# Optimization experiments

Measured on AMD Instinct MI355X. Metric: run time of the kernel, lower is better.

Reference implementation:

```python
import jax, jax.numpy as jnp
from jax import lax
import numpy as np

WIN = 9  # default window [9, 9] in the original module


def _box_sum(x, win):
    """Sum over a win x win window, stride 1, pad win//2 (same as conv2d with ones kernel).
    Implemented separably (two 1D convs) - mathematically identical to the 2D ones-kernel conv.
    x: [B, 1, H, W] float32.
    """
    pad = win // 2
    kh = jnp.ones((1, 1, win, 1), x.dtype)
    kw = jnp.ones((1, 1, 1, win), x.dtype)
    dn = lax.conv_dimension_numbers(x.shape, kh.shape, ('NCHW', 'OIHW', 'NCHW'))
    y = lax.conv_general_dilated(x, kh, (1, 1), [(pad, pad), (0, 0)], dimension_numbers=dn)
    return lax.conv_general_dilated(y, kw, (1, 1), [(0, 0), (pad, pad)], dimension_numbers=dn)


def setup_inputs() -> dict:
    key = jax.random.key(0)
    k1, k2 = jax.random.split(key)
    shape = (32, 1, 512, 512)
    predict = jax.random.uniform(k1, shape, dtype=jnp.float32)
    target = jax.random.uniform(k2, shape, dtype=jnp.float32)
    return {"predict": predict, "target": target}


def reference(predict, target):
    win = WIN
    win_size = jnp.asarray(win * win, jnp.float32)

    I, J = predict, target
    I_sum = _box_sum(I, win)
    J_sum = _box_sum(J, win)
    I2_sum = _box_sum(I * I, win)
    J2_sum = _box_sum(J * J, win)
    IJ_sum = _box_sum(I * J, win)

    u_I = I_sum / win_size
    u_J = J_sum / win_size

    cross = IJ_sum - u_J * I_sum - u_I * J_sum + u_I * u_J * win_size
    I_var = I2_sum - 2.0 * u_I * I_sum + u_I * u_I * win_size
    J_var = J2_sum - 2.0 * u_J * J_sum + u_J * u_J * win_size

    cc = cross * cross / (I_var * J_var + 1e-6)
    return -jnp.mean(cc) + 1.0
```

## Files before the change

### kernel.cpp

```cpp
#include <hip/hip_runtime.h>


#define W 512
#define H 512
#define BH 4
#define NBANDS (H / BH)
#define NT 256
#define WPB 4

__device__ __forceinline__ float4 ld4(const float* p) {
    return *reinterpret_cast<const float4*>(p);
}

#define VROW(row, OP)                                                        \
    do {                                                                     \
        const float* _ip = Ip + (row) * W + x0;                              \
        const float* _jp = Jp + (row) * W + x0;                              \
        float4 _A0 = ld4(_ip);                                               \
        float4 _A1 = ld4(_ip + 4);                                           \
        float4 _B0 = ld4(_jp);                                               \
        float4 _B1 = ld4(_jp + 4);                                           \
        float _a0 = _A0.x, _a1 = _A0.y, _a2 = _A0.z, _a3 = _A0.w;            \
        float _a4 = _A1.x, _a5 = _A1.y, _a6 = _A1.z, _a7 = _A1.w;            \
        float _b0 = _B0.x, _b1 = _B0.y, _b2 = _B0.z, _b3 = _B0.w;            \
        float _b4 = _B1.x, _b5 = _B1.y, _b6 = _B1.z, _b7 = _B1.w;            \
        v0[0] OP _a0; v0[1] OP _a1; v0[2] OP _a2; v0[3] OP _a3;              \
        v0[4] OP _a4; v0[5] OP _a5; v0[6] OP _a6; v0[7] OP _a7;              \
        v1[0] OP _b0; v1[1] OP _b1; v1[2] OP _b2; v1[3] OP _b3;              \
        v1[4] OP _b4; v1[5] OP _b5; v1[6] OP _b6; v1[7] OP _b7;              \
        v2[0] OP _a0*_a0; v2[1] OP _a1*_a1; v2[2] OP _a2*_a2; v2[3] OP _a3*_a3; \
        v2[4] OP _a4*_a4; v2[5] OP _a5*_a5; v2[6] OP _a6*_a6; v2[7] OP _a7*_a7; \
        v3[0] OP _b0*_b0; v3[1] OP _b1*_b1; v3[2] OP _b2*_b2; v3[3] OP _b3*_b3; \
        v3[4] OP _b4*_b4; v3[5] OP _b5*_b5; v3[6] OP _b6*_b6; v3[7] OP _b7*_b7; \
        v4[0] OP _a0*_b0; v4[1] OP _a1*_b1; v4[2] OP _a2*_b2; v4[3] OP _a3*_b3; \
        v4[4] OP _a4*_b4; v4[5] OP _a5*_b5; v4[6] OP _a6*_b6; v4[7] OP _a7*_b7; \
    } while (0)

#define HSUM(vv, h)                                                          \
    do {                                                                     \
        float _l4 = __shfl_up(vv[4], 1),  _l5 = __shfl_up(vv[5], 1);         \
        float _l6 = __shfl_up(vv[6], 1),  _l7 = __shfl_up(vv[7], 1);         \
        float _r0 = __shfl_down(vv[0], 1), _r1 = __shfl_down(vv[1], 1);      \
        float _r2 = __shfl_down(vv[2], 1), _r3 = __shfl_down(vv[3], 1);      \
        _l4 = lane ? _l4 : 0.f; _l5 = lane ? _l5 : 0.f;                      \
        _l6 = lane ? _l6 : 0.f; _l7 = lane ? _l7 : 0.f;                      \
        _r0 = lastl ? 0.f : _r0; _r1 = lastl ? 0.f : _r1;                    \
        _r2 = lastl ? 0.f : _r2; _r3 = lastl ? 0.f : _r3;                    \
        float _t = (((_l4 + _l5) + (_l6 + _l7)) +                            \
                    ((vv[0] + vv[1]) + (vv[2] + vv[3]))) + vv[4];            \
        h[0] = _t;                                                           \
        _t += vv[5] - _l4;  h[1] = _t;                                       \
        _t += vv[6] - _l5;  h[2] = _t;                                       \
        _t += vv[7] - _l6;  h[3] = _t;                                       \
        _t += _r0   - _l7;  h[4] = _t;                                       \
        _t += _r1 - vv[0];  h[5] = _t;                                       \
        _t += _r2 - vv[1];  h[6] = _t;                                       \
        _t += _r3 - vv[2];  h[7] = _t;                                       \
    } while (0)

__global__ __launch_bounds__(NT)
void ncc_main(const float* __restrict__ I, const float* __restrict__ J,
              float* __restrict__ partials) {
    const int lane  = threadIdx.x & 63;
    const bool lastl = (lane == 63);
    const int wid   = threadIdx.x >> 6;

    const int nblk = gridDim.x;
    const int sblk = (blockIdx.x & 7) * (nblk >> 3) + (blockIdx.x >> 3);

    const int g    = sblk * WPB + wid;
    const int b    = g >> 7;
    const int band = g & (NBANDS - 1);
    const int y0   = band * BH;
    const float* Ip = I + (size_t)b * (H * W);
    const float* Jp = J + (size_t)b * (H * W);
    const int x0 = lane * 8;

    float v0[8], v1[8], v2[8], v3[8], v4[8];
    #pragma unroll
    for (int k = 0; k < 8; ++k) { v0[k]=0.f; v1[k]=0.f; v2[k]=0.f; v3[k]=0.f; v4[k]=0.f; }

    #pragma unroll
    for (int dr = -4; dr < 4; ++dr) {
        int r = y0 + dr;
        if (r >= 0) VROW(r, +=);
    }

    float cc_acc = 0.f;
    const float inv81 = 1.f / 81.f;
    #pragma unroll
    for (int i = 0; i < BH; ++i) {
        const int y = y0 + i;
        if (y + 4 < H) VROW(y + 4, +=);

        float h0[8], h1[8], h2[8], h3[8], h4[8];
        HSUM(v0, h0);
        HSUM(v1, h1);
        HSUM(v2, h2);
        HSUM(v3, h3);
        HSUM(v4, h4);

        #pragma unroll
        for (int c = 0; c < 8; ++c) {
            float Is = h0[c], Js = h1[c];
            float I2 = h2[c], J2 = h3[c], IJ = h4[c];
            float u     = Is * inv81;
            float cross = IJ - u * Js;
            float Ivar  = I2 - u * Is;
            float Jvar  = J2 - (Js * inv81) * Js;
            float r     = __builtin_amdgcn_rcpf(Ivar * Jvar + 1e-6f);
            cc_acc += (cross * cross) * r;
        }

        if (y - 4 >= 0) VROW(y - 4, -=);
    }

    #pragma unroll
    for (int off = 32; off > 0; off >>= 1)
        cc_acc += __shfl_down(cc_acc, off, 64);
    __shared__ float wsum[WPB];
    if (lane == 0) wsum[wid] = cc_acc;
    __syncthreads();
    if (threadIdx.x == 0)
        partials[blockIdx.x] = (wsum[0] + wsum[1]) + (wsum[2] + wsum[3]);
}

__global__ __launch_bounds__(256)
void ncc_finish(const float* __restrict__ partials, float* __restrict__ out,
                int n, float inv_total) {
    float v = 0.f;
    for (int i = threadIdx.x; i < n; i += blockDim.x) v += partials[i];
    #pragma unroll
    for (int off = 32; off > 0; off >>= 1)
        v += __shfl_down(v, off, 64);
    __shared__ float wsum[4];
    if ((threadIdx.x & 63) == 0) wsum[threadIdx.x >> 6] = v;
    __syncthreads();
    if (threadIdx.x == 0) {
        float t = (wsum[0] + wsum[1]) + (wsum[2] + wsum[3]);
        out[0] = 1.0f - t * inv_total;
    }
}

extern "C" void kernel_launch(void* const* d_in, const int* in_sizes, int n_in,
                              void* d_out, int out_size, void* d_ws, size_t ws_size,
                              hipStream_t stream) {
    const float* I = (const float*)d_in[0];
    const float* J = (const float*)d_in[1];
    float* out = (float*)d_out;
    float* partials = (float*)d_ws;

    const int n = in_sizes[0];
    const int B = n / (H * W);
    const int nblocks = B * NBANDS / WPB;

    ncc_main<<<nblocks, NT, 0, stream>>>(I, J, partials);
    ncc_finish<<<1, 256, 0, stream>>>(partials, out, nblocks, 1.0f / (float)n);
}
```

Before: 120.0 us.

## Software-pipeline row loads with double buffers and split horizontal sum epilogue

Replaces the conditional per-row load-and-accumulate with an explicit two-buffer software pipeline, so the next row's global loads are issued before the current row is accumulated. Out-of-range rows are clamped to a valid address and masked by a sign multiplier instead of being skipped by a branch. The horizontal sliding sum is split into low and high halves so fewer temporaries stay live, and launch bounds now request 4 blocks per CU. This aims to hide memory latency and lower register pressure, at the cost of extra multiplies and redundant loads on boundary bands.

Result: faster. 116.8 us (-2.7%).

```diff
diff --git a/kernel.cpp b/kernel.cpp
--- a/kernel.cpp
+++ b/kernel.cpp
@@ -12,58 +12,87 @@
     return *reinterpret_cast<const float4*>(p);
 }
 
-#define VROW(row, OP)                                                        \
-    do {                                                                     \
-        const float* _ip = Ip + (row) * W + x0;                              \
-        const float* _jp = Jp + (row) * W + x0;                              \
-        float4 _A0 = ld4(_ip);                                               \
-        float4 _A1 = ld4(_ip + 4);                                           \
-        float4 _B0 = ld4(_jp);                                               \
-        float4 _B1 = ld4(_jp + 4);                                           \
-        float _a0 = _A0.x, _a1 = _A0.y, _a2 = _A0.z, _a3 = _A0.w;            \
-        float _a4 = _A1.x, _a5 = _A1.y, _a6 = _A1.z, _a7 = _A1.w;            \
-        float _b0 = _B0.x, _b1 = _B0.y, _b2 = _B0.z, _b3 = _B0.w;            \
-        float _b4 = _B1.x, _b5 = _B1.y, _b6 = _B1.z, _b7 = _B1.w;            \
-        v0[0] OP _a0; v0[1] OP _a1; v0[2] OP _a2; v0[3] OP _a3;              \
-        v0[4] OP _a4; v0[5] OP _a5; v0[6] OP _a6; v0[7] OP _a7;              \
-        v1[0] OP _b0; v1[1] OP _b1; v1[2] OP _b2; v1[3] OP _b3;              \
-        v1[4] OP _b4; v1[5] OP _b5; v1[6] OP _b6; v1[7] OP _b7;              \
-        v2[0] OP _a0*_a0; v2[1] OP _a1*_a1; v2[2] OP _a2*_a2; v2[3] OP _a3*_a3; \
-        v2[4] OP _a4*_a4; v2[5] OP _a5*_a5; v2[6] OP _a6*_a6; v2[7] OP _a7*_a7; \
-        v3[0] OP _b0*_b0; v3[1] OP _b1*_b1; v3[2] OP _b2*_b2; v3[3] OP _b3*_b3; \
-        v3[4] OP _b4*_b4; v3[5] OP _b5*_b5; v3[6] OP _b6*_b6; v3[7] OP _b7*_b7; \
-        v4[0] OP _a0*_b0; v4[1] OP _a1*_b1; v4[2] OP _a2*_b2; v4[3] OP _a3*_b3; \
-        v4[4] OP _a4*_b4; v4[5] OP _a5*_b5; v4[6] OP _a6*_b6; v4[7] OP _a7*_b7; \
-    } while (0)
+#define DECLBUF(P) float4 P##A0, P##A1, P##B0, P##B1; float P##m
 
-#define HSUM(vv, h)                                                          \
-    do {                                                                     \
-        float _l4 = __shfl_up(vv[4], 1),  _l5 = __shfl_up(vv[5], 1);         \
-        float _l6 = __shfl_up(vv[6], 1),  _l7 = __shfl_up(vv[7], 1);         \
-        float _r0 = __shfl_down(vv[0], 1), _r1 = __shfl_down(vv[1], 1);      \
-        float _r2 = __shfl_down(vv[2], 1), _r3 = __shfl_down(vv[3], 1);      \
-        _l4 = lane ? _l4 : 0.f; _l5 = lane ? _l5 : 0.f;                      \
-        _l6 = lane ? _l6 : 0.f; _l7 = lane ? _l7 : 0.f;                      \
-        _r0 = lastl ? 0.f : _r0; _r1 = lastl ? 0.f : _r1;                    \
-        _r2 = lastl ? 0.f : _r2; _r3 = lastl ? 0.f : _r3;                    \
-        float _t = (((_l4 + _l5) + (_l6 + _l7)) +                            \
-                    ((vv[0] + vv[1]) + (vv[2] + vv[3]))) + vv[4];            \
-        h[0] = _t;                                                           \
-        _t += vv[5] - _l4;  h[1] = _t;                                       \
-        _t += vv[6] - _l5;  h[2] = _t;                                       \
-        _t += vv[7] - _l6;  h[3] = _t;                                       \
-        _t += _r0   - _l7;  h[4] = _t;                                       \
-        _t += _r1 - vv[0];  h[5] = _t;                                       \
-        _t += _r2 - vv[1];  h[6] = _t;                                       \
-        _t += _r3 - vv[2];  h[7] = _t;                                       \
-    } while (0)
+#define PLOAD(P, DRK, SGNK) do {                                             \
+    int _r  = y0 + (DRK);                                                    \
+    int _rc = _r < 0 ? 0 : (_r > (H - 1) ? (H - 1) : _r);                    \
+    const float* _ip = Ip + _rc * W + x0;                                    \
+    const float* _jp = Jp + _rc * W + x0;                                    \
+    P##A0 = ld4(_ip);     P##A1 = ld4(_ip + 4);                              \
+    P##B0 = ld4(_jp);     P##B1 = ld4(_jp + 4);                              \
+    P##m  = (_r == _rc) ? (SGNK) : 0.f;                                      \
+} while (0)
 
-__global__ __launch_bounds__(NT)
+#define PACC(P) do {                                                         \
+    float _m = P##m;                                                         \
+    float _a0=P##A0.x*_m, _a1=P##A0.y*_m, _a2=P##A0.z*_m, _a3=P##A0.w*_m;    \
+    float _a4=P##A1.x*_m, _a5=P##A1.y*_m, _a6=P##A1.z*_m, _a7=P##A1.w*_m;    \
+    float _b0=P##B0.x*_m, _b1=P##B0.y*_m, _b2=P##B0.z*_m, _b3=P##B0.w*_m;    \
+    float _b4=P##B1.x*_m, _b5=P##B1.y*_m, _b6=P##B1.z*_m, _b7=P##B1.w*_m;    \
+    v0[0]+=_a0; v0[1]+=_a1; v0[2]+=_a2; v0[3]+=_a3;                          \
+    v0[4]+=_a4; v0[5]+=_a5; v0[6]+=_a6; v0[7]+=_a7;                          \
+    v1[0]+=_b0; v1[1]+=_b1; v1[2]+=_b2; v1[3]+=_b3;                          \
+    v1[4]+=_b4; v1[5]+=_b5; v1[6]+=_b6; v1[7]+=_b7;                          \
+    v2[0]+=_a0*P##A0.x; v2[1]+=_a1*P##A0.y; v2[2]+=_a2*P##A0.z; v2[3]+=_a3*P##A0.w; \
+    v2[4]+=_a4*P##A1.x; v2[5]+=_a5*P##A1.y; v2[6]+=_a6*P##A1.z; v2[7]+=_a7*P##A1.w; \
+    v3[0]+=_b0*P##B0.x; v3[1]+=_b1*P##B0.y; v3[2]+=_b2*P##B0.z; v3[3]+=_b3*P##B0.w; \
+    v3[4]+=_b4*P##B1.x; v3[5]+=_b5*P##B1.y; v3[6]+=_b6*P##B1.z; v3[7]+=_b7*P##B1.w; \
+    v4[0]+=_a0*P##B0.x; v4[1]+=_a1*P##B0.y; v4[2]+=_a2*P##B0.z; v4[3]+=_a3*P##B0.w; \
+    v4[4]+=_a4*P##B1.x; v4[5]+=_a5*P##B1.y; v4[6]+=_a6*P##B1.z; v4[7]+=_a7*P##B1.w; \
+} while (0)
+
+#define HLO(vv, h, l7out) do {                                               \
+    float _l4 = __shfl_up(vv[4], 1), _l5 = __shfl_up(vv[5], 1);              \
+    float _l6 = __shfl_up(vv[6], 1), _l7 = __shfl_up(vv[7], 1);              \
+    if (lane == 0) { _l4 = 0.f; _l5 = 0.f; _l6 = 0.f; _l7 = 0.f; }           \
+    float _t = (((_l4+_l5)+(_l6+_l7)) + ((vv[0]+vv[1])+(vv[2]+vv[3]))) + vv[4]; \
+    h[0] = _t;                                                               \
+    _t += vv[5] - _l4; h[1] = _t;                                            \
+    _t += vv[6] - _l5; h[2] = _t;                                            \
+    _t += vv[7] - _l6; h[3] = _t;                                            \
+    l7out = _l7;                                                             \
+} while (0)
+
+#define HHI(vv, h3in, l7in, h) do {                                          \
+    float _r0 = __shfl_down(vv[0], 1), _r1 = __shfl_down(vv[1], 1);          \
+    float _r2 = __shfl_down(vv[2], 1), _r3 = __shfl_down(vv[3], 1);          \
+    if (lane == 63) { _r0 = 0.f; _r1 = 0.f; _r2 = 0.f; _r3 = 0.f; }          \
+    float _t = (h3in) + _r0 - (l7in); h[0] = _t;                             \
+    _t += _r1 - vv[0]; h[1] = _t;                                            \
+    _t += _r2 - vv[1]; h[2] = _t;                                            \
+    _t += _r3 - vv[2]; h[3] = _t;                                            \
+} while (0)
+
+#define CC4(h0a, h1a, h2a, h3a, h4a) do {                                    \
+    _Pragma("unroll")                                                        \
+    for (int _c = 0; _c < 4; ++_c) {                                         \
+        float _Is = h0a[_c], _Js = h1a[_c];                                  \
+        float _u  = _Is * inv81;                                             \
+        float _cr = h4a[_c] - _u * _Js;                                      \
+        float _Iv = h2a[_c] - _u * _Is;                                      \
+        float _Jv = h3a[_c] - (_Js * inv81) * _Js;                           \
+        cc_acc += (_cr * _cr) * __builtin_amdgcn_rcpf(_Iv * _Jv + 1e-6f);    \
+    }                                                                        \
+} while (0)
+
+#define EPI() do {                                                           \
+    float h0[4], h1[4], h2[4], h3[4], h4[4];                                 \
+    float s0, s1, s2, s3, s4;                                                \
+    HLO(v0, h0, s0); HLO(v1, h1, s1); HLO(v2, h2, s2);                       \
+    HLO(v3, h3, s3); HLO(v4, h4, s4);                                        \
+    CC4(h0, h1, h2, h3, h4);                                                 \
+    float e0 = h0[3], e1 = h1[3], e2 = h2[3], e3 = h3[3], e4 = h4[3];        \
+    HHI(v0, e0, s0, h0); HHI(v1, e1, s1, h1); HHI(v2, e2, s2, h2);           \
+    HHI(v3, e3, s3, h3); HHI(v4, e4, s4, h4);                                \
+    CC4(h0, h1, h2, h3, h4);                                                 \
+} while (0)
+
+__global__ __launch_bounds__(NT, 4)
 void ncc_main(const float* __restrict__ I, const float* __restrict__ J,
               float* __restrict__ partials) {
-    const int lane  = threadIdx.x & 63;
-    const bool lastl = (lane == 63);
-    const int wid   = threadIdx.x >> 6;
+    const int lane = threadIdx.x & 63;
+    const int wid  = threadIdx.x >> 6;
 
     const int nblk = gridDim.x;
     const int sblk = (blockIdx.x & 7) * (nblk >> 3) + (blockIdx.x >> 3);
@@ -80,40 +109,32 @@
     #pragma unroll
     for (int k = 0; k < 8; ++k) { v0[k]=0.f; v1[k]=0.f; v2[k]=0.f; v3[k]=0.f; v4[k]=0.f; }
 
-    #pragma unroll
-    for (int dr = -4; dr < 4; ++dr) {
-        int r = y0 + dr;
-        if (r >= 0) VROW(r, +=);
-    }
-
     float cc_acc = 0.f;
     const float inv81 = 1.f / 81.f;
-    #pragma unroll
-    for (int i = 0; i < BH; ++i) {
-        const int y = y0 + i;
-        if (y + 4 < H) VROW(y + 4, +=);
 
-        float h0[8], h1[8], h2[8], h3[8], h4[8];
-        HSUM(v0, h0);
-        HSUM(v1, h1);
-        HSUM(v2, h2);
-        HSUM(v3, h3);
-        HSUM(v4, h4);
+    DECLBUF(p); DECLBUF(q);
 
-        #pragma unroll
-        for (int c = 0; c < 8; ++c) {
-            float Is = h0[c], Js = h1[c];
-            float I2 = h2[c], J2 = h3[c], IJ = h4[c];
-            float u     = Is * inv81;
-            float cross = IJ - u * Js;
-            float Ivar  = I2 - u * Is;
-            float Jvar  = J2 - (Js * inv81) * Js;
-            float r     = __builtin_amdgcn_rcpf(Ivar * Jvar + 1e-6f);
-            cc_acc += (cross * cross) * r;
-        }
-
-        if (y - 4 >= 0) VROW(y - 4, -=);
-    }
+    PLOAD(p, -4, 1.f);
+    PLOAD(q, -3, 1.f);
+    PACC(p); PLOAD(p, -2, 1.f);
+    PACC(q); PLOAD(q, -1, 1.f);
+    PACC(p); PLOAD(p,  0, 1.f);
+    PACC(q); PLOAD(q,  1, 1.f);
+    PACC(p); PLOAD(p,  2, 1.f);
+    PACC(q); PLOAD(q,  3, 1.f);
+    PACC(p); PLOAD(p,  4, 1.f);
+    PACC(q); PLOAD(q, -4, -1.f);
+    PACC(p); PLOAD(p,  5, 1.f);
+    EPI();
+    PACC(q); PLOAD(q, -3, -1.f);
+    PACC(p); PLOAD(p,  6, 1.f);
+    EPI();
+    PACC(q); PLOAD(q, -2, -1.f);
+    PACC(p); PLOAD(p,  7, 1.f);
+    EPI();
+    PACC(q);
+    PACC(p);
+    EPI();
 
     #pragma unroll
     for (int off = 32; off > 0; off >>= 1)
```
